# Kernel tuning notes

Hardware: AMD Instinct MI355X
Metric: run time of the kernel (lower is better)

Reference implementation:

```python
import jax, jax.numpy as jnp
import numpy as np

B, N, H = 8, 1024, 768
NH, HD = 12, 64  # num heads, head size
E = 131072       # total edges (avg degree 16)
N_REL = 30


def setup_inputs() -> dict:
    key = jax.random.key(0)
    ks = jax.random.split(key, 8)
    node_states = jax.random.normal(ks[0], (B, N, H), dtype=jnp.float32)
    eb = jax.random.randint(ks[1], (E,), 0, B, dtype=jnp.int32)
    ei = jax.random.randint(ks[2], (E,), 0, N, dtype=jnp.int32)
    ej = jax.random.randint(ks[3], (E,), 0, N, dtype=jnp.int32)
    er = jax.random.randint(ks[4], (E,), 0, N_REL, dtype=jnp.int32)
    edge_indices = jnp.stack([eb, ei, ej, er], axis=0)  # (4, E)
    scale = 1.0 / np.sqrt(H)
    Wq = jax.random.normal(ks[5], (H, H), dtype=jnp.float32) * scale
    Wk = jax.random.normal(ks[6], (H, H), dtype=jnp.float32) * scale
    Wv = jax.random.normal(ks[7], (H, H), dtype=jnp.float32) * scale
    return {"node_states": node_states, "edge_indices": edge_indices,
            "Wq": Wq, "Wk": Wk, "Wv": Wv}


def reference(node_states, edge_indices, Wq, Wk, Wv):
    # node_states: (B, N, H); edge_indices: (4, E) rows = (batch, head_node, tail_node, relation)
    b, i, j = edge_indices[0], edge_indices[1], edge_indices[2]
    q = (node_states @ Wq).reshape(B, N, NH, HD)
    k = (node_states @ Wk).reshape(B, N, NH, HD)
    v = (node_states @ Wv).reshape(B, N, NH, HD)
    qe = q[b, i]  # (E, NH, HD) gather at head nodes
    ke = k[b, j]  # (E, NH, HD) gather at tail nodes
    scores = jnp.einsum('ehd,ehd->eh', qe, ke) * (1.0 / np.sqrt(HD))  # (E, NH)
    seg = b * N + i  # segment = (batch, head_node)
    nseg = B * N
    smax = jax.ops.segment_max(scores, seg, num_segments=nseg)  # (nseg, NH)
    ex = jnp.exp(scores - smax[seg])
    denom = jax.ops.segment_sum(ex, seg, num_segments=nseg)
    probs = ex / jnp.maximum(denom[seg], 1e-9)  # (E, NH) edge softmax over tail nodes
    ve = v[b, j]  # (E, NH, HD)
    out_e = (probs[:, :, None] * ve).reshape(E, NH * HD)
    out = jax.ops.segment_sum(out_e, seg, num_segments=nseg)  # sum over tail dim
    return out.reshape(B, N, H)
```

## Files before the change

### kernel.cpp

```cpp
#include <hip/hip_runtime.h>
#include <hip/hip_fp16.h>

#define BB 8
#define NN 1024
#define HH 768
#define NHEAD 12
#define HD 64
#define NSEG 8192
#define QKVN 2304
#define MAXDEG 64

typedef unsigned short u16;
typedef __attribute__((ext_vector_type(8))) _Float16 f16x8;
typedef __attribute__((ext_vector_type(4))) float f32x4;
typedef __attribute__((ext_vector_type(4))) unsigned int u32x4;
typedef __attribute__((ext_vector_type(2))) unsigned int u32x2;

__device__ __forceinline__ u16 f2h(float f) {
  _Float16 h = (_Float16)f;
  return __builtin_bit_cast(u16, h);
}
__device__ __forceinline__ __half2 h2(unsigned int w) {
  return __builtin_bit_cast(__half2, w);
}

#define CAST_BLKS (NSEG * HH / 4 / 256)
#define TW_BLKS   ((QKVN / 32) * (HH / 32))
#define BUILD_BLKS 512

__global__ void prep_kernel(const float* __restrict__ X, u16* __restrict__ Xb,
                            const float* __restrict__ Wq, const float* __restrict__ Wk,
                            const float* __restrict__ Wv, u16* __restrict__ Wt,
                            const int* __restrict__ EI, int* __restrict__ cursor,
                            int* __restrict__ tailrow, int E) {
  const int bid = blockIdx.x;
  if (bid < CAST_BLKS) {
    int i = bid * 256 + threadIdx.x;
    float4 f = ((const float4*)X)[i];
    ushort4 o;
    o.x = f2h(f.x); o.y = f2h(f.y); o.z = f2h(f.z); o.w = f2h(f.w);
    ((ushort4*)Xb)[i] = o;
  } else if (bid < CAST_BLKS + TW_BLKS) {
    __shared__ float tile[32][33];
    int t = bid - CAST_BLKS;
    int n0 = (t % (QKVN / 32)) * 32;
    int k0 = (t / (QKVN / 32)) * 32;
    const float* W = (n0 < HH) ? Wq : (n0 < 2 * HH ? Wk : Wv);
    int nb = n0 - (n0 < HH ? 0 : (n0 < 2 * HH ? HH : 2 * HH));
    int tx = threadIdx.x & 31, ty = threadIdx.x >> 5;
#pragma unroll
    for (int r = 0; r < 4; ++r)
      tile[ty + 8 * r][tx] = W[(k0 + ty + 8 * r) * HH + nb + tx];
    __syncthreads();
#pragma unroll
    for (int r = 0; r < 4; ++r)
      Wt[(n0 + ty + 8 * r) * HH + k0 + tx] = f2h(tile[tx][ty + 8 * r]);
  } else {
    int e = (bid - CAST_BLKS - TW_BLKS) * 256 + threadIdx.x;
    if (e >= E) return;
    int b = EI[e];
    int seg = b * NN + EI[E + e];
    int j = EI[2 * E + e];
    int pos = atomicAdd(&cursor[seg], 1);
    if (pos < MAXDEG) tailrow[seg * MAXDEG + pos] = b * NN + j;
  }
}

#define BM 128
#define BN 128
#define BK 32
#define NITER (HH / BK)

__global__ __launch_bounds__(256) void gemm_kernel(const u16* __restrict__ Xb,
                                                   const u16* __restrict__ Wt,
                                                   u16* __restrict__ QKV) {
  __shared__ u16 As[3][BM * BK];
  __shared__ u16 Bs[3][BN * BK];
  const int tid = threadIdx.x;
  const int wave = tid >> 6;
  const int lane = tid & 63;
  const int bid = blockIdx.x;
  const int mt = (bid & 7) * 8 + ((bid >> 3) & 7);
  const int nt = bid >> 6;
  const int m0 = mt * BM;
  const int n0 = nt * BN;
  const int wr = wave >> 1;
  const int wc = wave & 1;
  const int quad = lane >> 4;
  const int l15 = lane & 15;

  f32x4 acc[4][4] = {};

  const int srow = wave * 16 + (lane >> 2);
  const int scol = (((lane & 3) ^ ((lane >> 3) & 3)) << 3);
  const int rswz = quad ^ ((l15 >> 1) & 3);

  auto stage = [&](int buf, int kt) {
#pragma unroll
    for (int p = 0; p < 2; ++p) {
      const u16* ga = Xb + (m0 + p * 64 + srow) * HH + kt + scol;
      const u16* gb = Wt + (n0 + p * 64 + srow) * HH + kt + scol;
      u16* la = As[buf] + p * 2048 + wave * 512;
      u16* lb = Bs[buf] + p * 2048 + wave * 512;
      __builtin_amdgcn_global_load_lds(
          (const __attribute__((address_space(1))) unsigned int*)(unsigned long long)ga,
          (__attribute__((address_space(3))) unsigned int*)(unsigned long long)la, 16, 0, 0);
      __builtin_amdgcn_global_load_lds(
          (const __attribute__((address_space(1))) unsigned int*)(unsigned long long)gb,
          (__attribute__((address_space(3))) unsigned int*)(unsigned long long)lb, 16, 0, 0);
    }
  };

  stage(0, 0);
  stage(1, BK);

#pragma unroll 3
  for (int it = 0; it < NITER; ++it) {
    if (it != NITER - 1) {
      asm volatile("s_waitcnt vmcnt(4)" ::: "memory");
    } else {
      asm volatile("s_waitcnt vmcnt(0)" ::: "memory");
    }
    asm volatile("s_barrier" ::: "memory");
    if (it + 2 < NITER) stage((it + 2) % 3, (it + 2) * BK);

    const int b = it % 3;
    f16x8 afr[4], bfr[4];
#pragma unroll
    for (int mi = 0; mi < 4; ++mi) {
      int m = wr * 64 + mi * 16 + l15;
      afr[mi] = *(const f16x8*)(As[b] + m * BK + rswz * 8);
    }
#pragma unroll
    for (int ni = 0; ni < 4; ++ni) {
      int n = wc * 64 + ni * 16 + l15;
      bfr[ni] = *(const f16x8*)(Bs[b] + n * BK + rswz * 8);
    }
#pragma unroll
    for (int mi = 0; mi < 4; ++mi)
#pragma unroll
      for (int ni = 0; ni < 4; ++ni)
        acc[mi][ni] = __builtin_amdgcn_mfma_f32_16x16x32_f16(afr[mi], bfr[ni], acc[mi][ni], 0, 0, 0);
  }

#pragma unroll
  for (int mi = 0; mi < 4; ++mi)
#pragma unroll
    for (int ni = 0; ni < 4; ++ni) {
      int col = n0 + wc * 64 + ni * 16 + l15;
#pragma unroll
      for (int r = 0; r < 4; ++r) {
        int row = m0 + wr * 64 + mi * 16 + quad * 4 + r;
        QKV[row * QKVN + col] = f2h(acc[mi][ni][r]);
      }
    }
}

__global__ __launch_bounds__(256) void attn_kernel(const u16* __restrict__ QKV,
                                                   const int* __restrict__ tailrow,
                                                   const int* __restrict__ cursor,
                                                   float* __restrict__ out) {
  __shared__ float sm[3 * 16 * 64];
  const int wv = threadIdx.x >> 6;
  const int lane = threadIdx.x & 63;
  const int seg = (blockIdx.x & 7) * (NSEG / 8) + (blockIdx.x >> 3);
  const int base = seg * MAXDEG;
  int cnt = cursor[seg];
  if (cnt > MAXDEG) cnt = MAXDEG;
  const int myn = (cnt > wv) ? ((cnt - wv + 3) >> 2) : 0;

  int myidx = (lane < cnt) ? tailrow[base + lane] : 0;

  const u16* qrow = QKV + seg * QKVN;
  __half2 q1[4], q2[2];
  {
    u32x4 qa = *(const u32x4*)(qrow + lane * 8);
    u32x2 qb = *(const u32x2*)(qrow + 512 + lane * 4);
    const __half2 sc = __float2half2_rn(0.125f);
#pragma unroll
    for (int i = 0; i < 4; ++i) q1[i] = __hmul2(h2(qa[i]), sc);
    q2[0] = __hmul2(h2(qb[0]), sc);
    q2[1] = __hmul2(h2(qb[1]), sc);
  }

  float m1 = -__builtin_inff(), l1 = 0.f;
  float m2 = -__builtin_inff(), l2 = 0.f;
  __half2 o1[4] = {}, o2[2] = {};

  auto loadkv = [&](int row, u32x4& k1, u32x2& k2, u32x4& v1, u32x2& v2) {
    const u16* kp = QKV + row * QKVN + HH;
    k1 = *(const u32x4*)(kp + lane * 8);
    k2 = *(const u32x2*)(kp + 512 + lane * 4);
    v1 = *(const u32x4*)(kp + HH + lane * 8);
    v2 = *(const u32x2*)(kp + HH + 512 + lane * 4);
  };

  auto process = [&](u32x4 k1, u32x2 k2, u32x4 v1, u32x2 v2) {
    __half2 a1 = __hmul2(q1[0], h2(k1[0]));
    a1 = __hfma2(q1[1], h2(k1[1]), a1);
    a1 = __hfma2(q1[2], h2(k1[2]), a1);
    a1 = __hfma2(q1[3], h2(k1[3]), a1);
    float s1 = __low2float(a1) + __high2float(a1);
    s1 += __shfl_xor(s1, 1, 64);
    s1 += __shfl_xor(s1, 2, 64);
    s1 += __shfl_xor(s1, 4, 64);
    __half2 a2 = __hmul2(q2[0], h2(k2[0]));
    a2 = __hfma2(q2[1], h2(k2[1]), a2);
    float s2 = __low2float(a2) + __high2float(a2);
    s2 += __shfl_xor(s2, 1, 64);
    s2 += __shfl_xor(s2, 2, 64);
    s2 += __shfl_xor(s2, 4, 64);
    s2 += __shfl_xor(s2, 8, 64);
    {
      float mn = fmaxf(m1, s1);
      float al = __expf(m1 - mn);
      float ex = __expf(s1 - mn);
      l1 = l1 * al + ex;
      __half2 ah = __float2half2_rn(al), eh = __float2half2_rn(ex);
#pragma unroll
      for (int i = 0; i < 4; ++i)
        o1[i] = __hfma2(o1[i], ah, __hmul2(h2(v1[i]), eh));
      m1 = mn;
    }
    {
      float mn = fmaxf(m2, s2);
      float al = __expf(m2 - mn);
      float ex = __expf(s2 - mn);
      l2 = l2 * al + ex;
      __half2 ah = __float2half2_rn(al), eh = __float2half2_rn(ex);
      o2[0] = __hfma2(o2[0], ah, __hmul2(h2(v2[0]), eh));
      o2[1] = __hfma2(o2[1], ah, __hmul2(h2(v2[1]), eh));
      m2 = mn;
    }
  };

  if (myn > 0) {
    u32x4 k1c, v1c, k1n, v1n, k1n2, v1n2;
    u32x2 k2c, v2c, k2n, v2n, k2n2, v2n2;
    loadkv(__shfl(myidx, wv, 64), k1c, k2c, v1c, v2c);
    if (myn > 1) loadkv(__shfl(myidx, wv + 4, 64), k1n, k2n, v1n, v2n);
    for (int t = 0; t < myn; ++t) {
      if (t + 2 < myn)
        loadkv(__shfl(myidx, wv + 4 * (t + 2), 64), k1n2, k2n2, v1n2, v2n2);
      process(k1c, k2c, v1c, v2c);
      k1c = k1n; k2c = k2n; v1c = v1n; v2c = v2n;
      k1n = k1n2; k2n = k2n2; v1n = v1n2; v2n = v2n2;
    }
  }

  float of1[8], of2[4];
#pragma unroll
  for (int i = 0; i < 4; ++i) {
    of1[2 * i] = __low2float(o1[i]);
    of1[2 * i + 1] = __high2float(o1[i]);
  }
#pragma unroll
  for (int i = 0; i < 2; ++i) {
    of2[2 * i] = __low2float(o2[i]);
    of2[2 * i + 1] = __high2float(o2[i]);
  }

  if (wv > 0) {
    float* sb = sm + (wv - 1) * 1024;
    sb[0 * 64 + lane] = m1;  sb[1 * 64 + lane] = l1;
    sb[2 * 64 + lane] = m2;  sb[3 * 64 + lane] = l2;
#pragma unroll
    for (int i = 0; i < 8; ++i) sb[(4 + i) * 64 + lane] = of1[i];
#pragma unroll
    for (int i = 0; i < 4; ++i) sb[(12 + i) * 64 + lane] = of2[i];
  }
  __syncthreads();
  if (wv == 0) {
    float mn1 = fmaxf(m1, -1e30f), mn2 = fmaxf(m2, -1e30f);
#pragma unroll
    for (int j = 0; j < 3; ++j) {
      mn1 = fmaxf(mn1, sm[j * 1024 + 0 * 64 + lane]);
      mn2 = fmaxf(mn2, sm[j * 1024 + 2 * 64 + lane]);
    }
    float res1[8], res2[4];
    {
      float a0 = __expf(m1 - mn1);
      float l = l1 * a0;
#pragma unroll
      for (int i = 0; i < 8; ++i) res1[i] = of1[i] * a0;
#pragma unroll
      for (int j = 0; j < 3; ++j) {
        const float* sb = sm + j * 1024;
        float aj = __expf(sb[0 * 64 + lane] - mn1);
        l += sb[1 * 64 + lane] * aj;
#pragma unroll
        for (int i = 0; i < 8; ++i) res1[i] += sb[(4 + i) * 64 + lane] * aj;
      }
      float inv = 1.f / fmaxf(l, 1e-9f);
#pragma unroll
      for (int i = 0; i < 8; ++i) res1[i] *= inv;
    }
    {
      float a0 = __expf(m2 - mn2);
      float l = l2 * a0;
#pragma unroll
      for (int i = 0; i < 4; ++i) res2[i] = of2[i] * a0;
#pragma unroll
      for (int j = 0; j < 3; ++j) {
        const float* sb = sm + j * 1024;
        float aj = __expf(sb[2 * 64 + lane] - mn2);
        l += sb[3 * 64 + lane] * aj;
#pragma unroll
        for (int i = 0; i < 4; ++i) res2[i] += sb[(12 + i) * 64 + lane] * aj;
      }
      float inv = 1.f / fmaxf(l, 1e-9f);
#pragma unroll
      for (int i = 0; i < 4; ++i) res2[i] *= inv;
    }

    float* op = out + seg * HH;
    float4 r0 = {res1[0], res1[1], res1[2], res1[3]};
    float4 r1 = {res1[4], res1[5], res1[6], res1[7]};
    float4 r2 = {res2[0], res2[1], res2[2], res2[3]};
    ((float4*)(op + lane * 8))[0] = r0;
    ((float4*)(op + lane * 8))[1] = r1;
    *(float4*)(op + 512 + lane * 4) = r2;
  }
}

extern "C" void kernel_launch(void* const* d_in, const int* in_sizes, int n_in,
                              void* d_out, int out_size, void* d_ws, size_t ws_size,
                              hipStream_t stream) {
  const float* X  = (const float*)d_in[0];
  const int*   EI = (const int*)d_in[1];
  const float* Wq = (const float*)d_in[2];
  const float* Wk = (const float*)d_in[3];
  const float* Wv = (const float*)d_in[4];
  float* out = (float*)d_out;
  const int E = in_sizes[1] / 4;

  char* ws = (char*)d_ws;
  int* cursor  = (int*)(ws);
  int* tailrow = (int*)(ws + 32768);
  u16* Xb      = (u16*)(ws + 2129920);
  u16* Wt      = (u16*)(ws + 14712832);
  u16* QKV     = (u16*)(ws + 18251776);

  hipMemsetAsync(cursor, 0, NSEG * 4, stream);
  prep_kernel<<<CAST_BLKS + TW_BLKS + BUILD_BLKS, 256, 0, stream>>>(
      X, Xb, Wq, Wk, Wv, Wt, EI, cursor, tailrow, E);
  gemm_kernel<<<(QKVN / BN) * (NSEG / BM), 256, 0, stream>>>(Xb, Wt, QKV);
  attn_kernel<<<NSEG, 256, 0, stream>>>(QKV, tailrow, cursor, out);
}
```

Measured before the change: 167.8 us.

## Enlarge QKV GEMM tiles to 256x128x64 with 8 waves and interleaved prefetch

The QKV projection GEMM now uses 256x128 output tiles with a K step of 64, run by 512 threads (8 waves) per block. It uses an XOR-swizzled LDS layout and splits each prefetch into two halves that are issued between the fragment loads of the two k-substeps. Extra barriers and s_setprio are added around the MFMA bursts, and blocks are remapped across XCDs. The aim is more data reuse per tile and better overlap of global loads with matrix math. In exchange it uses more LDS and registers per block and adds synchronisation.

```diff
diff --git a/kernel.cpp b/kernel.cpp
--- a/kernel.cpp
+++ b/kernel.cpp
@@ -66,91 +66,109 @@
   }
 }
 
-#define BM 128
-#define BN 128
-#define BK 32
-#define NITER (HH / BK)
-
-__global__ __launch_bounds__(256) void gemm_kernel(const u16* __restrict__ Xb,
-                                                   const u16* __restrict__ Wt,
-                                                   u16* __restrict__ QKV) {
-  __shared__ u16 As[3][BM * BK];
-  __shared__ u16 Bs[3][BN * BK];
+#define GBM 256
+#define GBN 128
+#define GBK 64
+#define GNT (HH / GBK)
+
+__global__ __launch_bounds__(512, 2) void gemm_kernel(const u16* __restrict__ Xb,
+                                                      const u16* __restrict__ Wt,
+                                                      u16* __restrict__ QKV) {
+  __shared__ u16 As[3][GBM * GBK];
+  __shared__ u16 Bs[3][GBN * GBK];
   const int tid = threadIdx.x;
   const int wave = tid >> 6;
   const int lane = tid & 63;
-  const int bid = blockIdx.x;
-  const int mt = (bid & 7) * 8 + ((bid >> 3) & 7);
-  const int nt = bid >> 6;
-  const int m0 = mt * BM;
-  const int n0 = nt * BN;
+  const int quad = lane >> 4;
+  const int l15 = lane & 15;
   const int wr = wave >> 1;
   const int wc = wave & 1;
-  const int quad = lane >> 4;
-  const int l15 = lane & 15;
+
+  const int bid = blockIdx.x;
+  const int wgid = (bid & 7) * 72 + (bid >> 3);
+  const int mt = wgid / 18;
+  const int nt = wgid % 18;
+  const int m0 = mt * GBM;
+  const int n0 = nt * GBN;
 
   f32x4 acc[4][4] = {};
 
-  const int srow = wave * 16 + (lane >> 2);
-  const int scol = (((lane & 3) ^ ((lane >> 3) & 3)) << 3);
-  const int rswz = quad ^ ((l15 >> 1) & 3);
-
-  auto stage = [&](int buf, int kt) {
-#pragma unroll
-    for (int p = 0; p < 2; ++p) {
-      const u16* ga = Xb + (m0 + p * 64 + srow) * HH + kt + scol;
-      const u16* gb = Wt + (n0 + p * 64 + srow) * HH + kt + scol;
-      u16* la = As[buf] + p * 2048 + wave * 512;
-      u16* lb = Bs[buf] + p * 2048 + wave * 512;
+  auto stage_half = [&](int buf, int kt, int h) {
+#pragma unroll
+    for (int iss = 0; iss < 2; ++iss) {
+      const int c = (wave * 4 + h * 2 + iss) * 64 + lane;
+      const int m = c >> 3;
+      const u16* ga = Xb + (m0 + m) * HH + kt + (((c & 7) ^ (m & 7)) << 3);
+      u16* la = &As[buf][c * 8];
       __builtin_amdgcn_global_load_lds(
           (const __attribute__((address_space(1))) unsigned int*)(unsigned long long)ga,
           (__attribute__((address_space(3))) unsigned int*)(unsigned long long)la, 16, 0, 0);
+    }
+    {
+      const int c = (wave * 2 + h) * 64 + lane;
+      const int n = c >> 3;
+      const u16* gb = Wt + (n0 + n) * HH + kt + (((c & 7) ^ (n & 7)) << 3);
+      u16* lb = &Bs[buf][c * 8];
       __builtin_amdgcn_global_load_lds(
           (const __attribute__((address_space(1))) unsigned int*)(unsigned long long)gb,
           (__attribute__((address_space(3))) unsigned int*)(unsigned long long)lb, 16, 0, 0);
     }
   };
 
-  stage(0, 0);
-  stage(1, BK);
+  stage_half(0, 0, 0);
+  stage_half(0, 0, 1);
+  stage_half(1, GBK, 0);
+  stage_half(1, GBK, 1);
 
 #pragma unroll 3
-  for (int it = 0; it < NITER; ++it) {
-    if (it != NITER - 1) {
-      asm volatile("s_waitcnt vmcnt(4)" ::: "memory");
+  for (int it = 0; it < GNT; ++it) {
+    if (it != GNT - 1) {
+      asm volatile("s_waitcnt vmcnt(6)" ::: "memory");
     } else {
       asm volatile("s_waitcnt vmcnt(0)" ::: "memory");
     }
-    asm volatile("s_barrier" ::: "memory");
-    if (it + 2 < NITER) stage((it + 2) % 3, (it + 2) * BK);
-
+    __builtin_amdgcn_s_barrier();
     const int b = it % 3;
-    f16x8 afr[4], bfr[4];
-#pragma unroll
-    for (int mi = 0; mi < 4; ++mi) {
-      int m = wr * 64 + mi * 16 + l15;
-      afr[mi] = *(const f16x8*)(As[b] + m * BK + rswz * 8);
-    }
+    const int nb2 = (it + 2) % 3;
+    const bool pre = (it + 2) < GNT;
+    const int ktn = (it + 2) * GBK;
+
+#pragma unroll
+    for (int ks = 0; ks < 2; ++ks) {
+      f16x8 afr[4], bfr[4];
+#pragma unroll
+      for (int mi = 0; mi < 4; ++mi) {
+        const int m = wr * 64 + mi * 16 + l15;
+        afr[mi] = *(const f16x8*)(&As[b][m * GBK + ((((ks << 2) | quad) ^ (m & 7)) << 3)]);
+      }
+#pragma unroll
+      for (int ni = 0; ni < 4; ++ni) {
+        const int n = wc * 64 + ni * 16 + l15;
+        bfr[ni] = *(const f16x8*)(&Bs[b][n * GBK + ((((ks << 2) | quad) ^ (n & 7)) << 3)]);
+      }
+      if (pre) stage_half(nb2, ktn, ks);
+      __builtin_amdgcn_s_barrier();
+      asm volatile("s_waitcnt lgkmcnt(0)" ::: "memory");
+      __builtin_amdgcn_sched_barrier(0);
+      __builtin_amdgcn_s_setprio(1);
+#pragma unroll
+      for (int mi = 0; mi < 4; ++mi)
+#pragma unroll
+        for (int ni = 0; ni < 4; ++ni)
+          acc[mi][ni] = __builtin_amdgcn_mfma_f32_16x16x32_f16(afr[mi], bfr[ni], acc[mi][ni], 0, 0, 0);
+      __builtin_amdgcn_s_setprio(0);
+      if (ks == 0) __builtin_amdgcn_s_barrier();
+    }
+  }
+
+#pragma unroll
+  for (int mi = 0; mi < 4; ++mi)
 #pragma unroll
     for (int ni = 0; ni < 4; ++ni) {
-      int n = wc * 64 + ni * 16 + l15;
-      bfr[ni] = *(const f16x8*)(Bs[b] + n * BK + rswz * 8);
-    }
-#pragma unroll
-    for (int mi = 0; mi < 4; ++mi)
-#pragma unroll
-      for (int ni = 0; ni < 4; ++ni)
-        acc[mi][ni] = __builtin_amdgcn_mfma_f32_16x16x32_f16(afr[mi], bfr[ni], acc[mi][ni], 0, 0, 0);
-  }
-
-#pragma unroll
-  for (int mi = 0; mi < 4; ++mi)
-#pragma unroll
-    for (int ni = 0; ni < 4; ++ni) {
-      int col = n0 + wc * 64 + ni * 16 + l15;
+      const int col = n0 + wc * 64 + ni * 16 + l15;
 #pragma unroll
       for (int r = 0; r < 4; ++r) {
-        int row = m0 + wr * 64 + mi * 16 + quad * 4 + r;
+        const int row = m0 + wr * 64 + mi * 16 + quad * 4 + r;
         QKV[row * QKVN + col] = f2h(acc[mi][ni][r]);
       }
     }
@@ -344,6 +362,6 @@
   hipMemsetAsync(cursor, 0, NSEG * 4, stream);
   prep_kernel<<<CAST_BLKS + TW_BLKS + BUILD_BLKS, 256, 0, stream>>>(
       X, Xb, Wq, Wk, Wv, Wt, EI, cursor, tailrow, E);
-  gemm_kernel<<<(QKVN / BN) * (NSEG / BM), 256, 0, stream>>>(Xb, Wt, QKV);
+  gemm_kernel<<<(NSEG / GBM) * (QKVN / GBN), 512, 0, stream>>>(Xb, Wt, QKV);
   attn_kernel<<<NSEG, 256, 0, stream>>>(QKV, tailrow, cursor, out);
 }
```

Measured after the change: 177.4 us. 1.06x slower.
